# Optimization experiments

Measured on AMD Instinct MI355X. Metric: run time of the kernel, lower is better.

## Reference

```python
import jax, jax.numpy as jnp
import numpy as np

H, D = 8, 64            # heads, per-head out feats (sect_dim/num_heads)
SENT_DIM, SECT_DIM = 256, 512
FFN_DIM = 2048
N_SENT, N_SECT = 100000, 20000
E1 = E2 = 320000
NEG_SLOPE = 0.2


def setup_inputs() -> dict:
    key = jax.random.key(0)
    ks = jax.random.split(key, 24)
    g = lambda i, shape, scale=0.05: jax.random.normal(ks[i], shape, jnp.float32) * scale
    inp = {
        "sent_repr": jax.random.normal(ks[0], (N_SENT, SENT_DIM), jnp.float32),
        "sect_repr": jax.random.normal(ks[1], (N_SECT, SECT_DIM), jnp.float32),
        "s2S_src": jax.random.randint(ks[2], (E1,), 0, N_SENT, jnp.int32),
        "s2S_dst": jax.random.randint(ks[3], (E1,), 0, N_SECT, jnp.int32),
        "S2S_src": jax.random.randint(ks[4], (E2,), 0, N_SECT, jnp.int32),
        "S2S_dst": jax.random.randint(ks[5], (E2,), 0, N_SECT, jnp.int32),
        # s2S GATConv (bipartite): separate src/dst projections
        "W1_src": g(6, (SENT_DIM, H * D)),
        "W1_dst": g(7, (SECT_DIM, H * D)),
        "al1": g(8, (H, D)),
        "ar1": g(9, (H, D)),
        "b1": g(10, (H * D,)),
        # S2S GATConv (homogeneous): single projection
        "W2": g(11, (SECT_DIM, H * D)),
        "al2": g(12, (H, D)),
        "ar2": g(13, (H, D)),
        "b2": g(14, (H * D,)),
        # Fusion gate
        "fus_w": g(15, (2 * SECT_DIM, 1)),
        "fus_b": g(16, (1,)),
        # FFN
        "ffn_w1": g(17, (SECT_DIM, FFN_DIM)),
        "ffn_b1": g(18, (FFN_DIM,)),
        "ffn_w2": g(19, (FFN_DIM, SECT_DIM)),
        "ffn_b2": g(20, (SECT_DIM,)),
    }
    return inp


def _gat(x_src, x_dst, W_src, W_dst, al, ar, bias, src, dst, n_dst):
    fs = (x_src @ W_src).reshape(-1, H, D)   # [N_src, H, D]
    fd = (x_dst @ W_dst).reshape(-1, H, D)   # [N_dst, H, D]
    el = jnp.einsum('nhd,hd->nh', fs, al)
    er = jnp.einsum('nhd,hd->nh', fd, ar)
    e = jax.nn.leaky_relu(el[src] + er[dst], NEG_SLOPE)          # [E, H]
    m = jax.ops.segment_max(e, dst, num_segments=n_dst)
    m = jnp.where(jnp.isfinite(m), m, 0.0)
    ex = jnp.exp(e - m[dst])                                     # [E, H]
    denom = jax.ops.segment_sum(ex, dst, num_segments=n_dst)     # [N_dst, H]
    msg = jax.ops.segment_sum(ex[:, :, None] * fs[src], dst, num_segments=n_dst)
    rst = msg / jnp.maximum(denom, 1e-9)[:, :, None]             # [N_dst, H, D]
    return rst + bias.reshape(1, H, D)


def reference(sent_repr, sect_repr, s2S_src, s2S_dst, S2S_src, S2S_dst,
              W1_src, W1_dst, al1, ar1, b1, W2, al2, ar2, b2,
              fus_w, fus_b, ffn_w1, ffn_b1, ffn_w2, ffn_b2):
    n = sect_repr.shape[0]
    s2S = jax.nn.elu(_gat(sent_repr, sect_repr, W1_src, W1_dst, al1, ar1, b1,
                          s2S_src, s2S_dst, n).reshape(n, -1))
    S2S = jax.nn.elu(_gat(sect_repr, sect_repr, W2, W2, al2, ar2, b2,
                          S2S_src, S2S_dst, n).reshape(n, -1))
    z = jax.nn.sigmoid(jnp.concatenate([s2S, S2S], axis=-1) @ fus_w + fus_b)  # [n,1]
    update = z * s2S + (1.0 - z) * S2S
    h = sect_repr + update
    return jax.nn.relu(h @ ffn_w1 + ffn_b1) @ ffn_w2 + ffn_b2
```

## Files before the change

kernel.cpp:

```cpp
#include <hip/hip_runtime.h>

#define E_EDGES 320000
#define NSENT   100000
#define NSENT_P 100096
#define NSECT   20000
#define NSECT_P 20096
#define SDIM    256
#define TDIM    512
#define FFN     2048
#define SENT_CONV_BLOCKS (NSENT_P * SDIM / 8 / 256)
#define SECT_CONV_BLOCKS (NSECT_P / 4)

typedef short bf16x8 __attribute__((ext_vector_type(8)));
typedef float f32x4  __attribute__((ext_vector_type(4)));

static __device__ __forceinline__ float bf2f(unsigned short u) {
    unsigned int i = ((unsigned int)u) << 16;
    float f; __builtin_memcpy(&f, &i, 4); return f;
}
static __device__ __forceinline__ unsigned short f2bf(float f) {
    unsigned int i; __builtin_memcpy(&i, &f, 4);
    unsigned int r = i + 0x7FFFu + ((i >> 16) & 1u);
    return (unsigned short)(r >> 16);
}

static __device__ __forceinline__ void gload16(const unsigned short* g, unsigned short* l) {
    __builtin_amdgcn_global_load_lds(
        (const __attribute__((address_space(1))) unsigned int*)g,
        (__attribute__((address_space(3))) unsigned int*)l, 16, 0, 0);
}

__global__ __launch_bounds__(256)
void k_prep(const float* __restrict__ W1d, const float* __restrict__ ar1, float* __restrict__ Wr1,
            const float* __restrict__ W1s, unsigned short* __restrict__ w1t,
            const float* __restrict__ W2,  unsigned short* __restrict__ w2t,
            const float* __restrict__ fw1, unsigned short* __restrict__ fw1t,
            const float* __restrict__ fw2, unsigned short* __restrict__ fw2t,
            int* __restrict__ cnt1, int* __restrict__ cnt2)
{
    int b = blockIdx.x, tid = threadIdx.x;
    if (b < 16) {
        int t = b * 256 + tid;
        int k = t >> 3, h = t & 7;
        float s = 0.f;
        for (int d = 0; d < 64; ++d) s += W1d[k * 512 + h * 64 + d] * ar1[h * 64 + d];
        Wr1[t] = s;
        return;
    }
    if (b >= 2448) {
        int zb = b - 2448;
        int idx = (zb < 79 ? zb : zb - 79) * 256 + tid;
        if (idx < NSECT) { if (zb < 79) cnt1[idx] = 0; else cnt2[idx] = 0; }
        return;
    }
    const float* in; unsigned short* out; int R, C, gx, local;
    if      (b < 144)  { local = b - 16;   in = W1s; out = w1t;  R = 256;  C = 512;  gx = 16; }
    else if (b < 400)  { local = b - 144;  in = W2;  out = w2t;  R = 512;  C = 512;  gx = 16; }
    else if (b < 1424) { local = b - 400;  in = fw1; out = fw1t; R = 512;  C = 2048; gx = 64; }
    else               { local = b - 1424; in = fw2; out = fw2t; R = 2048; C = 512;  gx = 16; }
    int bx = local % gx, by = local / gx;
    __shared__ float tile[32][33];
    int c0 = bx * 32, r0 = by * 32;
    int tx = tid & 31, ty = tid >> 5;
#pragma unroll
    for (int i = 0; i < 4; ++i)
        tile[ty + i * 8][tx] = in[(long)(r0 + ty + i * 8) * C + c0 + tx];
    __syncthreads();
#pragma unroll
    for (int i = 0; i < 4; ++i)
        out[(long)(c0 + ty + i * 8) * R + r0 + tx] = f2bf(tile[tx][ty + i * 8]);
}

__global__ __launch_bounds__(256)
void k_convert_all(const float* __restrict__ sent, unsigned short* __restrict__ sent_b,
                   const float* __restrict__ sect, unsigned short* __restrict__ sect_b,
                   const float* __restrict__ Wf, float* __restrict__ er1)
{
    int b = blockIdx.x, tid = threadIdx.x;
    if (b < SENT_CONV_BLOCKS) {
        long i8 = (((long)b * 256) + tid) * 8;
        int row = (int)(i8 >> 8);
        uint4 o;
        if (row < NSENT) {
            float4 v0 = *(const float4*)(sent + i8);
            float4 v1 = *(const float4*)(sent + i8 + 4);
            o.x = ((unsigned int)f2bf(v0.x)) | (((unsigned int)f2bf(v0.y)) << 16);
            o.y = ((unsigned int)f2bf(v0.z)) | (((unsigned int)f2bf(v0.w)) << 16);
            o.z = ((unsigned int)f2bf(v1.x)) | (((unsigned int)f2bf(v1.y)) << 16);
            o.w = ((unsigned int)f2bf(v1.z)) | (((unsigned int)f2bf(v1.w)) << 16);
        } else { o = make_uint4(0u, 0u, 0u, 0u); }
        *(uint4*)(sent_b + i8) = o;
        return;
    }
    int lane = tid & 63;
    int row  = (b - SENT_CONV_BLOCKS) * 4 + (tid >> 6);
    f32x4 w[16];
    const f32x4* wp = (const f32x4*)(Wf + lane * 64);
#pragma unroll
    for (int i = 0; i < 16; ++i) w[i] = wp[i];
    if (row >= NSECT_P) return;
    if (row >= NSECT) {
        *(uint4*)(sect_b + (long)row * TDIM + lane * 8) = make_uint4(0u, 0u, 0u, 0u);
        return;
    }
    float4 x0 = *(const float4*)(sect + (long)row * TDIM + lane * 8);
    float4 x1 = *(const float4*)(sect + (long)row * TDIM + lane * 8 + 4);
    uint4 o;
    o.x = ((unsigned int)f2bf(x0.x)) | (((unsigned int)f2bf(x0.y)) << 16);
    o.y = ((unsigned int)f2bf(x0.z)) | (((unsigned int)f2bf(x0.w)) << 16);
    o.z = ((unsigned int)f2bf(x1.x)) | (((unsigned int)f2bf(x1.y)) << 16);
    o.w = ((unsigned int)f2bf(x1.z)) | (((unsigned int)f2bf(x1.w)) << 16);
    *(uint4*)(sect_b + (long)row * TDIM + lane * 8) = o;

    float xs[8] = {x0.x, x0.y, x0.z, x0.w, x1.x, x1.y, x1.z, x1.w};
    float p[8] = {};
#pragma unroll
    for (int j = 0; j < 8; ++j) {
        f32x4 wa = w[j * 2], wb = w[j * 2 + 1];
        p[0] += xs[j] * wa[0]; p[1] += xs[j] * wa[1];
        p[2] += xs[j] * wa[2]; p[3] += xs[j] * wa[3];
        p[4] += xs[j] * wb[0]; p[5] += xs[j] * wb[1];
        p[6] += xs[j] * wb[2]; p[7] += xs[j] * wb[3];
    }
#pragma unroll
    for (int s = 1; s < 64; s <<= 1)
#pragma unroll
        for (int h = 0; h < 8; ++h) p[h] += __shfl_xor(p[h], s);
    if (lane == 0) {
        *(float4*)(er1 + (long)row * 8)     = make_float4(p[0], p[1], p[2], p[3]);
        *(float4*)(er1 + (long)row * 8 + 4) = make_float4(p[4], p[5], p[6], p[7]);
    }
}

template<int EPI, int NATT, int MT, int KU>
__global__ __launch_bounds__(256)
void k_gemm(const unsigned short* __restrict__ A, const unsigned short* __restrict__ BT,
            void* __restrict__ C, const float* __restrict__ bias,
            int N, int K, int Mreal, int ntx,
            const float* __restrict__ av0, float* __restrict__ eo0,
            const float* __restrict__ av1, float* __restrict__ eo1)
{
    __shared__ unsigned short a_s[KU][MT * 32][32];
    __shared__ unsigned short b_s[KU][128][32];
    const int tid  = threadIdx.x;
    const int lane = tid & 63;
    const int wid  = tid >> 6;
    const int wr   = (wid >> 1) * (16 * MT);
    const int wc   = (wid & 1) * 64;

    const int nwg = gridDim.x;
    const int bid = blockIdx.x;
    const int q = nwg >> 3, r = nwg & 7;
    const int xcd = bid & 7;
    const int wgid = (xcd < r ? xcd * (q + 1) : r * (q + 1) + (xcd - r) * q) + (bid >> 3);
    const int row0 = (wgid / ntx) * (32 * MT);
    const int col0 = (wgid % ntx) * 128;

    const int l4 = lane >> 2;
    const int lc = (lane & 3) * 8;

    const unsigned short* gA0;
    const unsigned short* gA1 = nullptr;
    if (MT == 2) {
        gA0 = A + (long)(row0 + 16 * wid + l4) * K + lc;
    } else {
        gA0 = A + (long)(row0 + 16 * (2 * wid) + l4) * K + lc;
        gA1 = A + (long)(row0 + 16 * (2 * wid + 1) + l4) * K + lc;
    }
    const unsigned short* gB0 = BT + (long)(col0 + 16 * (2 * wid) + l4) * K + lc;
    const unsigned short* gB1 = BT + (long)(col0 + 16 * (2 * wid + 1) + l4) * K + lc;

    f32x4 acc[MT][4] = {};

    for (int k0 = 0; k0 < K; k0 += 32 * KU) {
        __syncthreads();
#pragma unroll
        for (int u = 0; u < KU; ++u) {
            if (MT == 2) {
                gload16(gA0 + k0 + 32 * u, &a_s[u][16 * wid][0]);
            } else {
                gload16(gA0 + k0 + 32 * u, &a_s[u][32 * wid][0]);
                gload16(gA1 + k0 + 32 * u, &a_s[u][32 * wid + 16][0]);
            }
            gload16(gB0 + k0 + 32 * u, &b_s[u][32 * wid][0]);
            gload16(gB1 + k0 + 32 * u, &b_s[u][32 * wid + 16][0]);
        }
        __syncthreads();
#pragma unroll
        for (int u = 0; u < KU; ++u) {
            bf16x8 af[MT], bfr[4];
#pragma unroll
            for (int m = 0; m < MT; ++m)
                af[m] = *(const bf16x8*)&a_s[u][wr + m * 16 + (lane & 15)][8 * (lane >> 4)];
#pragma unroll
            for (int n = 0; n < 4; ++n)
                bfr[n] = *(const bf16x8*)&b_s[u][wc + n * 16 + (lane & 15)][8 * (lane >> 4)];
#pragma unroll
            for (int m = 0; m < MT; ++m)
#pragma unroll
                for (int n = 0; n < 4; ++n)
                    acc[m][n] = __builtin_amdgcn_mfma_f32_16x16x32_bf16(af[m], bfr[n], acc[m][n], 0, 0, 0);
        }
    }

#pragma unroll
    for (int m = 0; m < MT; ++m) {
        int row_t = wr + m * 16 + ((lane >> 4) << 2);
#pragma unroll
        for (int n = 0; n < 4; ++n) {
            int col = col0 + wc + n * 16 + (lane & 15);
#pragma unroll
            for (int r2 = 0; r2 < 4; ++r2) {
                int row = row0 + row_t + r2;
                float v = acc[m][n][r2];
                if (EPI >= 1) v += bias[col];
                if (EPI == 1) v = fmaxf(v, 0.f);
                if (EPI <= 1) {
                    ((unsigned short*)C)[(long)row * N + col] = f2bf(v);
                } else {
                    if (row < Mreal) ((float*)C)[(long)row * N + col] = v;
                }
            }
        }
    }

    if (NATT >= 1) {
        int hw = (col0 + wc) >> 6;
        float av0r[4], av1r[4];
#pragma unroll
        for (int n = 0; n < 4; ++n) {
            int c = col0 + wc + n * 16 + (lane & 15);
            av0r[n] = av0[c];
            if (NATT == 2) av1r[n] = av1[c];
        }
        float red0[MT * 4], red1[MT * 4];
#pragma unroll
        for (int m = 0; m < MT; ++m)
#pragma unroll
            for (int r2 = 0; r2 < 4; ++r2) {
                red0[m * 4 + r2] = acc[m][0][r2] * av0r[0] + acc[m][1][r2] * av0r[1]
                                 + acc[m][2][r2] * av0r[2] + acc[m][3][r2] * av0r[3];
                if (NATT == 2)
                    red1[m * 4 + r2] = acc[m][0][r2] * av1r[0] + acc[m][1][r2] * av1r[1]
                                     + acc[m][2][r2] * av1r[2] + acc[m][3][r2] * av1r[3];
            }
#pragma unroll
        for (int s = 1; s < 16; s <<= 1)
#pragma unroll
            for (int j = 0; j < MT * 4; ++j) {
                red0[j] += __shfl_xor(red0[j], s);
                if (NATT == 2) red1[j] += __shfl_xor(red1[j], s);
            }
        if ((lane & 15) == 0) {
#pragma unroll
            for (int m = 0; m < MT; ++m)
#pragma unroll
                for (int r2 = 0; r2 < 4; ++r2) {
                    int row = row0 + wr + m * 16 + ((lane >> 4) << 2) + r2;
                    eo0[row * 8 + hw] = red0[m * 4 + r2];
                    if (NATT == 2) eo1[row * 8 + hw] = red1[m * 4 + r2];
                }
        }
    }
}

__global__ void k_hist2(const int* __restrict__ dst1, int* __restrict__ cnt1,
                        const int* __restrict__ dst2, int* __restrict__ cnt2)
{
    int i = blockIdx.x * 256 + threadIdx.x;
    if (i < E_EDGES) atomicAdd(&cnt1[dst1[i]], 1);
    else             atomicAdd(&cnt2[dst2[i - E_EDGES]], 1);
}

__global__ void k_scan2(const int* __restrict__ cnt1, int* __restrict__ off1, int* __restrict__ cur1,
                        const int* __restrict__ cnt2, int* __restrict__ off2, int* __restrict__ cur2)
{
    const int* cnt = blockIdx.x ? cnt2 : cnt1;
    int* off = blockIdx.x ? off2 : off1;
    int* cur = blockIdx.x ? cur2 : cur1;
    __shared__ int partial[1024];
    int t = threadIdx.x;
    const int Nseg = NSECT;
    int chunk = (Nseg + 1023) / 1024;
    int b = t * chunk;
    int e_ = b + chunk; if (e_ > Nseg) e_ = Nseg; if (b > Nseg) b = Nseg;
    int s = 0;
    for (int i = b; i < e_; ++i) s += cnt[i];
    partial[t] = s;
    __syncthreads();
    for (int d = 1; d < 1024; d <<= 1) {
        int v = partial[t];
        int w = (t >= d) ? partial[t - d] : 0;
        __syncthreads();
        partial[t] = v + w;
        __syncthreads();
    }
    int run = (t == 0) ? 0 : partial[t - 1];
    for (int i = b; i < e_; ++i) { off[i] = run; cur[i] = run; run += cnt[i]; }
    if (t == 1023) off[Nseg] = partial[1023];
}

__global__ void k_scatter2(const int* __restrict__ src1, const int* __restrict__ dst1,
                           int* __restrict__ cur1, int* __restrict__ srcs1,
                           const int* __restrict__ src2, const int* __restrict__ dst2,
                           int* __restrict__ cur2, int* __restrict__ srcs2)
{
    int i = blockIdx.x * 256 + threadIdx.x;
    if (i < E_EDGES) {
        int p = atomicAdd(&cur1[dst1[i]], 1);
        srcs1[p] = src1[i];
    } else {
        int j = i - E_EDGES;
        int p = atomicAdd(&cur2[dst2[j]], 1);
        srcs2[p] = src2[j];
    }
}

static __device__ __forceinline__ void agg_core(
    const unsigned short* __restrict__ fs, const float* __restrict__ el,
    const float* __restrict__ er, const float* __restrict__ bias,
    const int* __restrict__ off, const int* __restrict__ srcs,
    int n, int lane, float o[8])
{
    int h8 = lane & 7;
    int beg = off[n], end = off[n + 1];
    float er_h = er[n * 8 + h8];

    float mx = -3.0e38f;
    for (int p = beg + (lane >> 3); p < end; p += 8) {
        int s = srcs[p];
        float e = el[s * 8 + h8] + er_h;
        e = (e >= 0.f) ? e : 0.2f * e;
        mx = fmaxf(mx, e);
    }
    mx = fmaxf(mx, __shfl_xor(mx, 8));
    mx = fmaxf(mx, __shfl_xor(mx, 16));
    mx = fmaxf(mx, __shfl_xor(mx, 32));

    int hc = lane >> 3;
    float mx_c = __shfl(mx, hc);
    float er_c = er[n * 8 + hc];

    float a0=0,a1=0,a2=0,a3=0,a4=0,a5=0,a6=0,a7=0,sw=0;
    const unsigned short* fsl = fs + lane * 8;

#define ACC8(vv, ww)                                                   \
    a0 += (ww) * bf2f((unsigned short)((vv).x & 0xFFFF));              \
    a1 += (ww) * bf2f((unsigned short)((vv).x >> 16));                 \
    a2 += (ww) * bf2f((unsigned short)((vv).y & 0xFFFF));              \
    a3 += (ww) * bf2f((unsigned short)((vv).y >> 16));                 \
    a4 += (ww) * bf2f((unsigned short)((vv).z & 0xFFFF));              \
    a5 += (ww) * bf2f((unsigned short)((vv).z >> 16));                 \
    a6 += (ww) * bf2f((unsigned short)((vv).w & 0xFFFF));              \
    a7 += (ww) * bf2f((unsigned short)((vv).w >> 16));

#define WCOMP(gg) ({ float e_ = (gg) + er_c; e_ = (e_ >= 0.f) ? e_ : 0.2f * e_; __expf(e_ - mx_c); })

    int p = beg;
    for (; p + 8 <= end; p += 8) {
        int s0 = srcs[p+0], s1 = srcs[p+1], s2 = srcs[p+2], s3 = srcs[p+3];
        int s4 = srcs[p+4], s5 = srcs[p+5], s6 = srcs[p+6], s7 = srcs[p+7];
        float g0 = el[s0*8+hc], g1 = el[s1*8+hc], g2 = el[s2*8+hc], g3 = el[s3*8+hc];
        float g4 = el[s4*8+hc], g5 = el[s5*8+hc], g6 = el[s6*8+hc], g7 = el[s7*8+hc];
        uint4 v0 = *(const uint4*)(fsl + (long)s0 * 512);
        uint4 v1 = *(const uint4*)(fsl + (long)s1 * 512);
        uint4 v2 = *(const uint4*)(fsl + (long)s2 * 512);
        uint4 v3 = *(const uint4*)(fsl + (long)s3 * 512);
        uint4 v4 = *(const uint4*)(fsl + (long)s4 * 512);
        uint4 v5 = *(const uint4*)(fsl + (long)s5 * 512);
        uint4 v6 = *(const uint4*)(fsl + (long)s6 * 512);
        uint4 v7 = *(const uint4*)(fsl + (long)s7 * 512);
        float w0 = WCOMP(g0), w1 = WCOMP(g1), w2 = WCOMP(g2), w3 = WCOMP(g3);
        float w4 = WCOMP(g4), w5 = WCOMP(g5), w6 = WCOMP(g6), w7 = WCOMP(g7);
        sw += w0 + w1 + w2 + w3 + w4 + w5 + w6 + w7;
        ACC8(v0, w0); ACC8(v1, w1); ACC8(v2, w2); ACC8(v3, w3);
        ACC8(v4, w4); ACC8(v5, w5); ACC8(v6, w6); ACC8(v7, w7);
    }
    for (; p < end; ++p) {
        int s = srcs[p];
        float gg = el[s * 8 + hc];
        uint4 v = *(const uint4*)(fsl + (long)s * 512);
        float ww = WCOMP(gg);
        sw += ww;
        ACC8(v, ww);
    }
#undef WCOMP
#undef ACC8

    float inv = 1.f / fmaxf(sw, 1e-9f);
    const float* bp = bias + lane * 8;
    o[0] = a0*inv + bp[0]; o[1] = a1*inv + bp[1]; o[2] = a2*inv + bp[2]; o[3] = a3*inv + bp[3];
    o[4] = a4*inv + bp[4]; o[5] = a5*inv + bp[5]; o[6] = a6*inv + bp[6]; o[7] = a7*inv + bp[7];
#pragma unroll
    for (int j = 0; j < 8; ++j) o[j] = (o[j] > 0.f) ? o[j] : (__expf(o[j]) - 1.f);
}

__global__ __launch_bounds__(256)
void k_agg_both(const unsigned short* __restrict__ fs1, const float* __restrict__ el1,
                const float* __restrict__ er1, const float* __restrict__ b1,
                const int* __restrict__ off1, const int* __restrict__ srcs1,
                const unsigned short* __restrict__ f2, const float* __restrict__ el2,
                const float* __restrict__ er2, const float* __restrict__ b2,
                const int* __restrict__ off2, const int* __restrict__ srcs2,
                const float* __restrict__ sect, const float* __restrict__ fw,
                const float* __restrict__ fb, unsigned short* __restrict__ hout)
{
    int n = blockIdx.x * 4 + (threadIdx.x >> 6);
    int lane = threadIdx.x & 63;
    if (n >= NSECT_P) return;
    long base = (long)n * TDIM + lane * 8;
    if (n >= NSECT) {
        *(uint4*)(hout + base) = make_uint4(0u, 0u, 0u, 0u);
        return;
    }
    float o1[8], o2[8];
    agg_core(fs1, el1, er1, b1, off1, srcs1, n, lane, o1);
    agg_core(f2,  el2, er2, b2, off2, srcs2, n, lane, o2);

    float4 wa0 = *(const float4*)(fw + lane * 8);
    float4 wa1 = *(const float4*)(fw + lane * 8 + 4);
    float4 wb0 = *(const float4*)(fw + 512 + lane * 8);
    float4 wb1 = *(const float4*)(fw + 512 + lane * 8 + 4);
    float part = o1[0]*wa0.x + o1[1]*wa0.y + o1[2]*wa0.z + o1[3]*wa0.w
               + o1[4]*wa1.x + o1[5]*wa1.y + o1[6]*wa1.z + o1[7]*wa1.w
               + o2[0]*wb0.x + o2[1]*wb0.y + o2[2]*wb0.z + o2[3]*wb0.w
               + o2[4]*wb1.x + o2[5]*wb1.y + o2[6]*wb1.z + o2[7]*wb1.w;
#pragma unroll
    for (int s = 1; s < 64; s <<= 1) part += __shfl_xor(part, s);
    float z = 1.f / (1.f + __expf(-(part + fb[0])));
    float4 r0 = *(const float4*)(sect + base);
    float4 r1 = *(const float4*)(sect + base + 4);
    float hv[8];
    hv[0] = r0.x + z * o1[0] + (1.f - z) * o2[0];
    hv[1] = r0.y + z * o1[1] + (1.f - z) * o2[1];
    hv[2] = r0.z + z * o1[2] + (1.f - z) * o2[2];
    hv[3] = r0.w + z * o1[3] + (1.f - z) * o2[3];
    hv[4] = r1.x + z * o1[4] + (1.f - z) * o2[4];
    hv[5] = r1.y + z * o1[5] + (1.f - z) * o2[5];
    hv[6] = r1.z + z * o1[6] + (1.f - z) * o2[6];
    hv[7] = r1.w + z * o1[7] + (1.f - z) * o2[7];
    uint4 u;
    u.x = ((unsigned int)f2bf(hv[0])) | (((unsigned int)f2bf(hv[1])) << 16);
    u.y = ((unsigned int)f2bf(hv[2])) | (((unsigned int)f2bf(hv[3])) << 16);
    u.z = ((unsigned int)f2bf(hv[4])) | (((unsigned int)f2bf(hv[5])) << 16);
    u.w = ((unsigned int)f2bf(hv[6])) | (((unsigned int)f2bf(hv[7])) << 16);
    *(uint4*)(hout + base) = u;
}

extern "C" void kernel_launch(void* const* d_in, const int* in_sizes, int n_in,
                              void* d_out, int out_size, void* d_ws, size_t ws_size,
                              hipStream_t stream)
{
    (void)in_sizes; (void)n_in; (void)out_size; (void)ws_size;
    const float* sent    = (const float*)d_in[0];
    const float* sect    = (const float*)d_in[1];
    const int*   s2S_src = (const int*)d_in[2];
    const int*   s2S_dst = (const int*)d_in[3];
    const int*   S2S_src = (const int*)d_in[4];
    const int*   S2S_dst = (const int*)d_in[5];
    const float* W1_src  = (const float*)d_in[6];
    const float* W1_dst  = (const float*)d_in[7];
    const float* al1     = (const float*)d_in[8];
    const float* ar1     = (const float*)d_in[9];
    const float* b1      = (const float*)d_in[10];
    const float* W2      = (const float*)d_in[11];
    const float* al2     = (const float*)d_in[12];
    const float* ar2     = (const float*)d_in[13];
    const float* b2      = (const float*)d_in[14];
    const float* fus_w   = (const float*)d_in[15];
    const float* fus_b   = (const float*)d_in[16];
    const float* ffn_w1  = (const float*)d_in[17];
    const float* ffn_b1  = (const float*)d_in[18];
    const float* ffn_w2  = (const float*)d_in[19];
    const float* ffn_b2  = (const float*)d_in[20];

    char* ws = (char*)d_ws;
    size_t curo = 0;
    auto alloc = [&](size_t sz) -> void* {
        void* p = ws + curo; curo += (sz + 255) & ~(size_t)255; return p;
    };

    unsigned short* sent_b = (unsigned short*)alloc((size_t)NSENT_P * SDIM * 2);
    unsigned short* sect_b = (unsigned short*)alloc((size_t)NSECT_P * TDIM * 2);
    unsigned short* w1t    = (unsigned short*)alloc((size_t)512 * 256 * 2);
    unsigned short* w2t    = (unsigned short*)alloc((size_t)512 * 512 * 2);
    unsigned short* fw1t   = (unsigned short*)alloc((size_t)2048 * 512 * 2);
    unsigned short* fw2t   = (unsigned short*)alloc((size_t)512 * 2048 * 2);
    float* Wr1 = (float*)alloc(512 * 8 * 4);
    float* el1 = (float*)alloc((size_t)NSENT_P * 8 * 4);
    float* er1 = (float*)alloc((size_t)NSECT_P * 8 * 4);
    float* el2 = (float*)alloc((size_t)NSECT_P * 8 * 4);
    float* er2 = (float*)alloc((size_t)NSECT_P * 8 * 4);
    unsigned short* fs1 = (unsigned short*)alloc((size_t)NSENT_P * 512 * 2);
    unsigned short* f2  = (unsigned short*)alloc((size_t)NSECT_P * 512 * 2);
    int* cnt1 = (int*)alloc((size_t)NSECT * 4);
    int* cnt2 = (int*)alloc((size_t)NSECT * 4);
    int* off1 = (int*)alloc((size_t)(NSECT + 1) * 4);
    int* off2 = (int*)alloc((size_t)(NSECT + 1) * 4);
    int* cur1 = (int*)alloc((size_t)NSECT * 4);
    int* cur2 = (int*)alloc((size_t)NSECT * 4);
    int* srcs1 = (int*)alloc((size_t)E_EDGES * 4);
    int* srcs2 = (int*)alloc((size_t)E_EDGES * 4);
    unsigned short* hb = (unsigned short*)alloc((size_t)NSECT_P * TDIM * 2);
    unsigned short* tb = fs1;

    k_prep<<<2606, 256, 0, stream>>>(W1_dst, ar1, Wr1, W1_src, w1t, W2, w2t,
                                     ffn_w1, fw1t, ffn_w2, fw2t, cnt1, cnt2);

    k_convert_all<<<SENT_CONV_BLOCKS + SECT_CONV_BLOCKS, 256, 0, stream>>>(
        sent, sent_b, sect, sect_b, Wr1, er1);

    k_gemm<0, 1, 4, 2><<<(NSENT_P / 128) * 4, 256, 0, stream>>>(sent_b, w1t, fs1, nullptr, 512, 256, 0, 4, al1, el1, nullptr, nullptr);
    k_gemm<0, 2, 2, 2><<<(NSECT_P / 64) * 4, 256, 0, stream>>>(sect_b, w2t, f2,  nullptr, 512, 512, 0, 4, al2, el2, ar2, er2);

    k_hist2<<<2 * E_EDGES / 256, 256, 0, stream>>>(s2S_dst, cnt1, S2S_dst, cnt2);
    k_scan2<<<2, 1024, 0, stream>>>(cnt1, off1, cur1, cnt2, off2, cur2);
    k_scatter2<<<2 * E_EDGES / 256, 256, 0, stream>>>(s2S_src, s2S_dst, cur1, srcs1,
                                                      S2S_src, S2S_dst, cur2, srcs2);

    k_agg_both<<<NSECT_P / 4, 256, 0, stream>>>(fs1, el1, er1, b1, off1, srcs1,
                                                f2, el2, er2, b2, off2, srcs2,
                                                sect, fus_w, fus_b, hb);

    k_gemm<1, 0, 4, 2><<<(NSECT_P / 128) * (FFN / 128), 256, 0, stream>>>(hb, fw1t, tb, ffn_b1, FFN, 512, 0, FFN / 128, nullptr, nullptr, nullptr, nullptr);
    k_gemm<2, 0, 2, 2><<<(NSECT_P / 64) * 4, 256, 0, stream>>>(tb, fw2t, d_out, ffn_b2, 512, FFN, NSECT, 4, nullptr, nullptr, nullptr, nullptr);
}
```

Baseline: 500.4 us.

## Split the two graph aggregations across separate waves and shrink the edge unroll

The fused aggregation kernel now gives each destination node two waves, one per graph (sentence-to-section and section-to-section). The second wave hands its result to the first through shared memory, and the first wave then applies the fusion gate. This doubles the number of waves in flight so more of the random gather latency can be hidden, at the cost of a block barrier and extra blocks. The inner edge loop is also unrolled by 4 instead of 8 to lower register pressure and raise occupancy.

```diff
diff --git a/kernel.cpp b/kernel.cpp
--- a/kernel.cpp
+++ b/kernel.cpp
@@ -354,37 +354,31 @@
     a6 += (ww) * bf2f((unsigned short)((vv).w & 0xFFFF));              \
     a7 += (ww) * bf2f((unsigned short)((vv).w >> 16));
 
-#define WCOMP(gg) ({ float e_ = (gg) + er_c; e_ = (e_ >= 0.f) ? e_ : 0.2f * e_; __expf(e_ - mx_c); })
-
     int p = beg;
-    for (; p + 8 <= end; p += 8) {
-        int s0 = srcs[p+0], s1 = srcs[p+1], s2 = srcs[p+2], s3 = srcs[p+3];
-        int s4 = srcs[p+4], s5 = srcs[p+5], s6 = srcs[p+6], s7 = srcs[p+7];
-        float g0 = el[s0*8+hc], g1 = el[s1*8+hc], g2 = el[s2*8+hc], g3 = el[s3*8+hc];
-        float g4 = el[s4*8+hc], g5 = el[s5*8+hc], g6 = el[s6*8+hc], g7 = el[s7*8+hc];
+    for (; p + 4 <= end; p += 4) {
+        int s0 = srcs[p + 0], s1 = srcs[p + 1], s2 = srcs[p + 2], s3 = srcs[p + 3];
+        float g0 = el[s0 * 8 + hc], g1 = el[s1 * 8 + hc];
+        float g2 = el[s2 * 8 + hc], g3 = el[s3 * 8 + hc];
         uint4 v0 = *(const uint4*)(fsl + (long)s0 * 512);
         uint4 v1 = *(const uint4*)(fsl + (long)s1 * 512);
         uint4 v2 = *(const uint4*)(fsl + (long)s2 * 512);
         uint4 v3 = *(const uint4*)(fsl + (long)s3 * 512);
-        uint4 v4 = *(const uint4*)(fsl + (long)s4 * 512);
-        uint4 v5 = *(const uint4*)(fsl + (long)s5 * 512);
-        uint4 v6 = *(const uint4*)(fsl + (long)s6 * 512);
-        uint4 v7 = *(const uint4*)(fsl + (long)s7 * 512);
-        float w0 = WCOMP(g0), w1 = WCOMP(g1), w2 = WCOMP(g2), w3 = WCOMP(g3);
-        float w4 = WCOMP(g4), w5 = WCOMP(g5), w6 = WCOMP(g6), w7 = WCOMP(g7);
-        sw += w0 + w1 + w2 + w3 + w4 + w5 + w6 + w7;
+        float e0 = g0 + er_c; e0 = (e0 >= 0.f) ? e0 : 0.2f * e0; float w0 = __expf(e0 - mx_c);
+        float e1 = g1 + er_c; e1 = (e1 >= 0.f) ? e1 : 0.2f * e1; float w1 = __expf(e1 - mx_c);
+        float e2 = g2 + er_c; e2 = (e2 >= 0.f) ? e2 : 0.2f * e2; float w2 = __expf(e2 - mx_c);
+        float e3 = g3 + er_c; e3 = (e3 >= 0.f) ? e3 : 0.2f * e3; float w3 = __expf(e3 - mx_c);
+        sw += w0 + w1 + w2 + w3;
         ACC8(v0, w0); ACC8(v1, w1); ACC8(v2, w2); ACC8(v3, w3);
-        ACC8(v4, w4); ACC8(v5, w5); ACC8(v6, w6); ACC8(v7, w7);
     }
     for (; p < end; ++p) {
         int s = srcs[p];
-        float gg = el[s * 8 + hc];
+        float e = el[s * 8 + hc] + er_c;
+        e = (e >= 0.f) ? e : 0.2f * e;
+        float ww0 = __expf(e - mx_c);
+        sw += ww0;
         uint4 v = *(const uint4*)(fsl + (long)s * 512);
-        float ww = WCOMP(gg);
-        sw += ww;
-        ACC8(v, ww);
-    }
-#undef WCOMP
+        ACC8(v, ww0);
+    }
 #undef ACC8
 
     float inv = 1.f / fmaxf(sw, 1e-9f);
@@ -405,17 +399,35 @@
                 const float* __restrict__ sect, const float* __restrict__ fw,
                 const float* __restrict__ fb, unsigned short* __restrict__ hout)
 {
-    int n = blockIdx.x * 4 + (threadIdx.x >> 6);
+    __shared__ float sh_o2[2][512];
+    int wid  = threadIdx.x >> 6;
     int lane = threadIdx.x & 63;
-    if (n >= NSECT_P) return;
+    int nloc = wid >> 1;
+    int graph = wid & 1;
+    int n = blockIdx.x * 2 + nloc;
+    bool real = (n < NSECT);
+
+    float o1[8];
+    if (real) {
+        if (graph == 0) {
+            agg_core(fs1, el1, er1, b1, off1, srcs1, n, lane, o1);
+        } else {
+            float o2[8];
+            agg_core(f2, el2, er2, b2, off2, srcs2, n, lane, o2);
+            *(float4*)&sh_o2[nloc][lane * 8]     = make_float4(o2[0], o2[1], o2[2], o2[3]);
+            *(float4*)&sh_o2[nloc][lane * 8 + 4] = make_float4(o2[4], o2[5], o2[6], o2[7]);
+        }
+    }
+    __syncthreads();
+    if (graph != 0) return;
     long base = (long)n * TDIM + lane * 8;
-    if (n >= NSECT) {
+    if (!real) {
         *(uint4*)(hout + base) = make_uint4(0u, 0u, 0u, 0u);
         return;
     }
-    float o1[8], o2[8];
-    agg_core(fs1, el1, er1, b1, off1, srcs1, n, lane, o1);
-    agg_core(f2,  el2, er2, b2, off2, srcs2, n, lane, o2);
+    float4 q0 = *(const float4*)&sh_o2[nloc][lane * 8];
+    float4 q1 = *(const float4*)&sh_o2[nloc][lane * 8 + 4];
+    float o2[8] = {q0.x, q0.y, q0.z, q0.w, q1.x, q1.y, q1.z, q1.w};
 
     float4 wa0 = *(const float4*)(fw + lane * 8);
     float4 wa1 = *(const float4*)(fw + lane * 8 + 4);
@@ -518,7 +530,7 @@
     k_scatter2<<<2 * E_EDGES / 256, 256, 0, stream>>>(s2S_src, s2S_dst, cur1, srcs1,
                                                       S2S_src, S2S_dst, cur2, srcs2);
 
-    k_agg_both<<<NSECT_P / 4, 256, 0, stream>>>(fs1, el1, er1, b1, off1, srcs1,
+    k_agg_both<<<NSECT_P / 2, 256, 0, stream>>>(fs1, el1, er1, b1, off1, srcs1,
                                                 f2, el2, er2, b2, off2, srcs2,
                                                 sect, fus_w, fus_b, hb);
 
```

After: 498.6 us. About the same (-0.4%).
